# Performance work log

Measured on AMD Instinct MI355X. Metric: run time of the kernel, lower is better.

Reference implementation:

```python
import math
import jax, jax.numpy as jnp
import numpy as np

K_NEIGH = 8  # module's self.k

def setup_inputs() -> dict:
    key = jax.random.key(0)
    ks = jax.random.split(key, 5)
    B, N, D = 4, 4096, 256
    s = 1.0 / math.sqrt(D)
    return {
        "x": jax.random.normal(ks[0], (B, N, D), dtype=jnp.float32),
        "Wqkv": jax.random.normal(ks[1], (3 * D, D), dtype=jnp.float32) * s,
        "bqkv": jax.random.normal(ks[2], (3 * D,), dtype=jnp.float32) * 0.02,
        "Wout": jax.random.normal(ks[3], (D, D), dtype=jnp.float32) * s,
        "bout": jax.random.normal(ks[4], (D,), dtype=jnp.float32) * 0.02,
    }

def reference(x, Wqkv, bqkv, Wout, bout):
    B, N, D = x.shape
    qkv = x @ Wqkv.T + bqkv                      # [B,N,3D]
    q, k, v = jnp.split(qkv, 3, axis=-1)         # each [B,N,D]
    # F.normalize(k, dim=-1) with eps=1e-12
    kn = k / jnp.maximum(jnp.linalg.norm(k, axis=-1, keepdims=True), 1e-12)
    sim = jnp.einsum('bnd,bmd->bnm', kn, kn)     # [B,N,N] cosine similarity
    sim = sim - 1e9 * jnp.eye(N, dtype=sim.dtype)
    k_val = min(K_NEIGH, N - 1)
    _, idx = jax.lax.top_k(sim, k_val)           # [B,N,k] neighbor indices
    # NOTE: the torch code builds k.unsqueeze(2).expand(B,N,N,D) and gathers on
    # dim 2, but that tensor is CONSTANT along dim 2, so the gather reduces to a
    # broadcast of k (and v) over the neighbor axis -- reproduced faithfully:
    k_sel = jnp.broadcast_to(k[:, :, None, :], (B, N, k_val, D))
    v_sel = jnp.broadcast_to(v[:, :, None, :], (B, N, k_val, D))
    scores = jnp.sum(q[:, :, None, :] * k_sel, axis=-1) / math.sqrt(D)  # [B,N,k]
    attn = jax.nn.softmax(scores, axis=-1)
    out = jnp.sum(attn[..., None] * v_sel, axis=2)                      # [B,N,D]
    return x + out @ Wout.T + bout
```

## Files before the change

kernel.cpp:

```cpp
#include <hip/hip_runtime.h>
#include <hip/hip_bf16.h>

#define DD 256
#define NROWS 16384
#define TILES 4
#define TROWS 16

typedef float f32x4 __attribute__((ext_vector_type(4)));
typedef __bf16 bf16x4 __attribute__((ext_vector_type(4)));
typedef __bf16 bf16x8 __attribute__((ext_vector_type(8)));

__device__ __forceinline__ bf16x8 cvt8(f32x4 lo, f32x4 hi) {
  bf16x8 v;
#pragma unroll
  for (int j = 0; j < 4; ++j) {
    v[j] = (__bf16)lo[j];
    v[4 + j] = (__bf16)hi[j];
  }
  return v;
}

__global__ __launch_bounds__(1024) void wc_bc_kernel(
    const float* __restrict__ Wqkv, const float* __restrict__ bqkv,
    const float* __restrict__ Wout, const float* __restrict__ bout,
    __bf16* __restrict__ Wc, float* __restrict__ bc) {
  __shared__ f32x4 part[16][64];
  __shared__ float red[4];
  const int i = blockIdx.x;
  const int t = threadIdx.x;
  const int w = t >> 6, l = t & 63;
  const float* __restrict__ Wv = Wqkv + 2 * DD * DD;
  const float* __restrict__ bv = bqkv + 2 * DD;
  const float* __restrict__ wrow = Wout + (size_t)i * DD;

  f32x4 wr[4];
#pragma unroll
  for (int k = 0; k < 4; ++k) wr[k] = *(const f32x4*)(wrow + w * 16 + k * 4);

  const float* wvp = Wv + (size_t)(w * 16) * DD + l * 4;
  f32x4 a0 = {0.f, 0.f, 0.f, 0.f}, a1 = {0.f, 0.f, 0.f, 0.f};
  f32x4 a2 = {0.f, 0.f, 0.f, 0.f}, a3 = {0.f, 0.f, 0.f, 0.f};
#pragma unroll
  for (int k = 0; k < 4; ++k) {
    a0 += wr[k][0] * *(const f32x4*)(wvp + (size_t)(4 * k + 0) * DD);
    a1 += wr[k][1] * *(const f32x4*)(wvp + (size_t)(4 * k + 1) * DD);
    a2 += wr[k][2] * *(const f32x4*)(wvp + (size_t)(4 * k + 2) * DD);
    a3 += wr[k][3] * *(const f32x4*)(wvp + (size_t)(4 * k + 3) * DD);
  }
  part[w][l] = (a0 + a1) + (a2 + a3);

  if (t < 256) {
    float p = wrow[t] * bv[t];
#pragma unroll
    for (int off = 32; off > 0; off >>= 1) p += __shfl_down(p, off);
    if (l == 0) red[w] = p;
  }
  __syncthreads();
  if (w == 0) {
    f32x4 s = {0.f, 0.f, 0.f, 0.f};
#pragma unroll
    for (int k = 0; k < 16; ++k) s += part[k][l];
    bf16x4 o;
#pragma unroll
    for (int j = 0; j < 4; ++j) o[j] = (__bf16)s[j];
    *(bf16x4*)(Wc + (size_t)i * DD + l * 4) = o;
    if (l == 0) bc[i] = bout[i] + red[0] + red[1] + red[2] + red[3];
  }
}

__global__ __launch_bounds__(256, 4) void knn_attn_main(
    const float* __restrict__ x, const __bf16* __restrict__ Wc,
    const float* __restrict__ bc, float* __restrict__ out) {
  __shared__ __bf16 xs[2][TROWS * DD];

  const int t = threadIdx.x;
  const int w = t >> 6, l = t & 63;
  const int cg = blockIdx.x >> 8;
  const int rb = blockIdx.x & 255;
  const int C0 = cg * 64;
  const int Rbase = rb * (TILES * TROWS);

  const int xrow = l & 15, g4 = l >> 4;
  const int rsw = (xrow & 7) << 4;
  const int rA = w * 16 + xrow;
  const int ocol = C0 + w * 16 + g4 * 4;

  bf16x8 af[8];
  {
    const __bf16* wrp = Wc + (size_t)(C0 + rA) * DD + g4 * 8;
#pragma unroll
    for (int ks = 0; ks < 8; ++ks) af[ks] = *(const bf16x8*)(wrp + ks * 32);
  }
  const f32x4 bias = *(const f32x4*)(bc + ocol);

  const int sr = t >> 4, sc = t & 15;
  const int ssw = (sr & 7) << 4;
  const int sbase = sr * 512 + sc * 32;

  {
    const float* s0 = x + (size_t)(Rbase + sr) * DD + sc * 16;
    f32x4 a = *(const f32x4*)(s0 + 0);
    f32x4 b = *(const f32x4*)(s0 + 4);
    f32x4 c = *(const f32x4*)(s0 + 8);
    f32x4 d = *(const f32x4*)(s0 + 12);
    char* xb = (char*)&xs[0][0];
    *(bf16x8*)(xb + ((sbase + 0) ^ ssw)) = cvt8(a, b);
    *(bf16x8*)(xb + ((sbase + 16) ^ ssw)) = cvt8(c, d);
  }
  __syncthreads();

  for (int i = 0; i < TILES; ++i) {
    f32x4 a, b, c, d;
    if (i + 1 < TILES) {
      const float* sn =
          x + (size_t)(Rbase + (i + 1) * TROWS + sr) * DD + sc * 16;
      a = *(const f32x4*)(sn + 0);
      b = *(const f32x4*)(sn + 4);
      c = *(const f32x4*)(sn + 8);
      d = *(const f32x4*)(sn + 12);
    }

    const char* xb = (const char*)&xs[i & 1][0];
    f32x4 acc = {0.f, 0.f, 0.f, 0.f};
#pragma unroll
    for (int ks = 0; ks < 8; ++ks) {
      const int kb = ks * 64 + g4 * 16;
      bf16x8 bfr = *(const bf16x8*)(xb + ((xrow * 512 + kb) ^ rsw));
      acc = __builtin_amdgcn_mfma_f32_16x16x32_bf16(af[ks], bfr, acc, 0, 0, 0);
    }
    {
      const size_t idx = (size_t)(Rbase + i * TROWS + xrow) * DD + ocol;
      f32x4 xres = *(const f32x4*)(x + idx);
      *(f32x4*)(out + idx) = acc + xres + bias;
    }

    if (i + 1 < TILES) {
      char* xbn = (char*)&xs[(i + 1) & 1][0];
      *(bf16x8*)(xbn + ((sbase + 0) ^ ssw)) = cvt8(a, b);
      *(bf16x8*)(xbn + ((sbase + 16) ^ ssw)) = cvt8(c, d);
    }
    __syncthreads();
  }
}

extern "C" void kernel_launch(void* const* d_in, const int* in_sizes, int n_in,
                              void* d_out, int out_size, void* d_ws, size_t ws_size,
                              hipStream_t stream) {
  const float* x = (const float*)d_in[0];
  const float* Wqkv = (const float*)d_in[1];
  const float* bqkv = (const float*)d_in[2];
  const float* Wout = (const float*)d_in[3];
  const float* bout = (const float*)d_in[4];
  float* out = (float*)d_out;

  __bf16* Wc = (__bf16*)d_ws;
  float* bc = (float*)((char*)d_ws + DD * DD * sizeof(__bf16));

  wc_bc_kernel<<<DD, 1024, 0, stream>>>(Wqkv, bqkv, Wout, bout, Wc, bc);
  knn_attn_main<<<1024, 256, 0, stream>>>(x, Wc, bc, out);
}
```

Measured before the change: 23.14 us.

## Take residual from bf16 LDS tile, halve tiles per block, batch weight-fold rows

The main kernel now takes the residual x from the bf16 copy already staged in shared memory, so x is no longer read a second time from global memory in fp32. Each block processes two 16-row tiles instead of four, which doubles the grid, and launch bounds are raised to allow more resident blocks. The staging loads are rearranged so adjacent threads read adjacent 32-byte chunks. The weight-folding kernel computes four output rows per block with 64 blocks. The cost is that the residual is rounded to bf16, which adds error to the output and risks the accuracy tolerance.

```diff
diff --git a/kernel.cpp b/kernel.cpp
--- a/kernel.cpp
+++ b/kernel.cpp
@@ -3,7 +3,7 @@
 
 #define DD 256
 #define NROWS 16384
-#define TILES 4
+#define TILES 2
 #define TROWS 16
 
 typedef float f32x4 __attribute__((ext_vector_type(4)));
@@ -24,59 +24,70 @@
     const float* __restrict__ Wqkv, const float* __restrict__ bqkv,
     const float* __restrict__ Wout, const float* __restrict__ bout,
     __bf16* __restrict__ Wc, float* __restrict__ bc) {
-  __shared__ f32x4 part[16][64];
+  __shared__ f32x4 part[16][4][64];
   __shared__ float red[4];
-  const int i = blockIdx.x;
+  const int i0 = blockIdx.x * 4;
   const int t = threadIdx.x;
   const int w = t >> 6, l = t & 63;
   const float* __restrict__ Wv = Wqkv + 2 * DD * DD;
   const float* __restrict__ bv = bqkv + 2 * DD;
-  const float* __restrict__ wrow = Wout + (size_t)i * DD;
 
-  f32x4 wr[4];
+  f32x4 wrc[4][4];
 #pragma unroll
-  for (int k = 0; k < 4; ++k) wr[k] = *(const f32x4*)(wrow + w * 16 + k * 4);
+  for (int r = 0; r < 4; ++r)
+#pragma unroll
+    for (int kk = 0; kk < 4; ++kk)
+      wrc[r][kk] = *(const f32x4*)(Wout + (size_t)(i0 + r) * DD + w * 16 + kk * 4);
 
   const float* wvp = Wv + (size_t)(w * 16) * DD + l * 4;
   f32x4 a0 = {0.f, 0.f, 0.f, 0.f}, a1 = {0.f, 0.f, 0.f, 0.f};
   f32x4 a2 = {0.f, 0.f, 0.f, 0.f}, a3 = {0.f, 0.f, 0.f, 0.f};
 #pragma unroll
-  for (int k = 0; k < 4; ++k) {
-    a0 += wr[k][0] * *(const f32x4*)(wvp + (size_t)(4 * k + 0) * DD);
-    a1 += wr[k][1] * *(const f32x4*)(wvp + (size_t)(4 * k + 1) * DD);
-    a2 += wr[k][2] * *(const f32x4*)(wvp + (size_t)(4 * k + 2) * DD);
-    a3 += wr[k][3] * *(const f32x4*)(wvp + (size_t)(4 * k + 3) * DD);
+  for (int k = 0; k < 16; ++k) {
+    f32x4 wv = *(const f32x4*)(wvp + (size_t)k * DD);
+    a0 += wv * wrc[0][k >> 2][k & 3];
+    a1 += wv * wrc[1][k >> 2][k & 3];
+    a2 += wv * wrc[2][k >> 2][k & 3];
+    a3 += wv * wrc[3][k >> 2][k & 3];
   }
-  part[w][l] = (a0 + a1) + (a2 + a3);
+  part[w][0][l] = a0;
+  part[w][1][l] = a1;
+  part[w][2][l] = a2;
+  part[w][3][l] = a3;
 
-  if (t < 256) {
-    float p = wrow[t] * bv[t];
+  if (t >= 256 && t < 512) {
+    const int r = (t >> 6) - 4, ll = t & 63;
+    float p = 0.f;
+#pragma unroll
+    for (int k = 0; k < 4; ++k)
+      p += Wout[(size_t)(i0 + r) * DD + k * 64 + ll] * bv[k * 64 + ll];
 #pragma unroll
     for (int off = 32; off > 0; off >>= 1) p += __shfl_down(p, off);
-    if (l == 0) red[w] = p;
+    if (ll == 0) red[r] = p;
   }
   __syncthreads();
-  if (w == 0) {
+  if (t < 256) {
+    const int r = t >> 6, q = t & 63;
     f32x4 s = {0.f, 0.f, 0.f, 0.f};
 #pragma unroll
-    for (int k = 0; k < 16; ++k) s += part[k][l];
+    for (int k = 0; k < 16; ++k) s += part[k][r][q];
     bf16x4 o;
 #pragma unroll
     for (int j = 0; j < 4; ++j) o[j] = (__bf16)s[j];
-    *(bf16x4*)(Wc + (size_t)i * DD + l * 4) = o;
-    if (l == 0) bc[i] = bout[i] + red[0] + red[1] + red[2] + red[3];
+    *(bf16x4*)(Wc + (size_t)(i0 + r) * DD + q * 4) = o;
   }
+  if (t < 4) bc[i0 + t] = bout[i0 + t] + red[t];
 }
 
-__global__ __launch_bounds__(256, 4) void knn_attn_main(
+__global__ __launch_bounds__(256, 6) void knn_attn_main(
     const float* __restrict__ x, const __bf16* __restrict__ Wc,
     const float* __restrict__ bc, float* __restrict__ out) {
   __shared__ __bf16 xs[2][TROWS * DD];
 
   const int t = threadIdx.x;
   const int w = t >> 6, l = t & 63;
-  const int cg = blockIdx.x >> 8;
-  const int rb = blockIdx.x & 255;
+  const int cg = blockIdx.x >> 9;
+  const int rb = blockIdx.x & 511;
   const int C0 = cg * 64;
   const int Rbase = rb * (TILES * TROWS);
 
@@ -95,29 +106,28 @@
 
   const int sr = t >> 4, sc = t & 15;
   const int ssw = (sr & 7) << 4;
-  const int sbase = sr * 512 + sc * 32;
+  const int cb0 = sr * 512 + sc * 16;
 
   {
-    const float* s0 = x + (size_t)(Rbase + sr) * DD + sc * 16;
-    f32x4 a = *(const f32x4*)(s0 + 0);
-    f32x4 b = *(const f32x4*)(s0 + 4);
-    f32x4 c = *(const f32x4*)(s0 + 8);
-    f32x4 d = *(const f32x4*)(s0 + 12);
+    const float* src = x + (size_t)(Rbase + sr) * DD + sc * 8;
+    f32x4 a = *(const f32x4*)(src);
+    f32x4 b = *(const f32x4*)(src + 4);
+    f32x4 c = *(const f32x4*)(src + 128);
+    f32x4 d = *(const f32x4*)(src + 132);
     char* xb = (char*)&xs[0][0];
-    *(bf16x8*)(xb + ((sbase + 0) ^ ssw)) = cvt8(a, b);
-    *(bf16x8*)(xb + ((sbase + 16) ^ ssw)) = cvt8(c, d);
+    *(bf16x8*)(xb + ((cb0 + 0) ^ ssw)) = cvt8(a, b);
+    *(bf16x8*)(xb + ((cb0 + 256) ^ ssw)) = cvt8(c, d);
   }
   __syncthreads();
 
   for (int i = 0; i < TILES; ++i) {
     f32x4 a, b, c, d;
     if (i + 1 < TILES) {
-      const float* sn =
-          x + (size_t)(Rbase + (i + 1) * TROWS + sr) * DD + sc * 16;
-      a = *(const f32x4*)(sn + 0);
+      const float* sn = x + (size_t)(Rbase + (i + 1) * TROWS + sr) * DD + sc * 8;
+      a = *(const f32x4*)(sn);
       b = *(const f32x4*)(sn + 4);
-      c = *(const f32x4*)(sn + 8);
-      d = *(const f32x4*)(sn + 12);
+      c = *(const f32x4*)(sn + 128);
+      d = *(const f32x4*)(sn + 132);
     }
 
     const char* xb = (const char*)&xs[i & 1][0];
@@ -129,15 +139,18 @@
       acc = __builtin_amdgcn_mfma_f32_16x16x32_bf16(af[ks], bfr, acc, 0, 0, 0);
     }
     {
-      const size_t idx = (size_t)(Rbase + i * TROWS + xrow) * DD + ocol;
-      f32x4 xres = *(const f32x4*)(x + idx);
-      *(f32x4*)(out + idx) = acc + xres + bias;
+      bf16x4 xr4 = *(const bf16x4*)(xb + ((xrow * 512 + ocol * 2) ^ rsw));
+      f32x4 xres;
+#pragma unroll
+      for (int j = 0; j < 4; ++j) xres[j] = (float)xr4[j];
+      *(f32x4*)(out + (size_t)(Rbase + i * TROWS + xrow) * DD + ocol) =
+          acc + xres + bias;
     }
 
     if (i + 1 < TILES) {
       char* xbn = (char*)&xs[(i + 1) & 1][0];
-      *(bf16x8*)(xbn + ((sbase + 0) ^ ssw)) = cvt8(a, b);
-      *(bf16x8*)(xbn + ((sbase + 16) ^ ssw)) = cvt8(c, d);
+      *(bf16x8*)(xbn + ((cb0 + 0) ^ ssw)) = cvt8(a, b);
+      *(bf16x8*)(xbn + ((cb0 + 256) ^ ssw)) = cvt8(c, d);
     }
     __syncthreads();
   }
@@ -156,6 +169,6 @@
   __bf16* Wc = (__bf16*)d_ws;
   float* bc = (float*)((char*)d_ws + DD * DD * sizeof(__bf16));
 
-  wc_bc_kernel<<<DD, 1024, 0, stream>>>(Wqkv, bqkv, Wout, bout, Wc, bc);
-  knn_attn_main<<<1024, 256, 0, stream>>>(x, Wc, bc, out);
+  wc_bc_kernel<<<64, 1024, 0, stream>>>(Wqkv, bqkv, Wout, bout, Wc, bc);
+  knn_attn_main<<<2048, 256, 0, stream>>>(x, Wc, bc, out);
 }
```

New measurement: 24.95 us. +7.9%, slower.

## Compute all output columns per block and take residual from shared tile

Applied to the files above, without the earlier changes.

Each block now covers all 256 output columns, with each wave holding four 16-column weight fragments in registers. This replaces the four column-group blocks that each re-staged the same x rows. The x fragments are loaded from LDS once per tile and reused across four MFMA chains. The residual is read from the bf16 LDS copy instead of the fp32 global x, which removes a second global read but rounds the residual to bf16. Register pressure rises, and the grid shrinks to 512 blocks with two tiles each.

```diff
diff --git a/kernel.cpp b/kernel.cpp
--- a/kernel.cpp
+++ b/kernel.cpp
@@ -3,7 +3,7 @@
 
 #define DD 256
 #define NROWS 16384
-#define TILES 4
+#define TILES 2
 #define TROWS 16
 
 typedef float f32x4 __attribute__((ext_vector_type(4)));
@@ -68,30 +68,27 @@
   }
 }
 
-__global__ __launch_bounds__(256, 4) void knn_attn_main(
+__global__ __launch_bounds__(256, 2) void knn_attn_main(
     const float* __restrict__ x, const __bf16* __restrict__ Wc,
     const float* __restrict__ bc, float* __restrict__ out) {
   __shared__ __bf16 xs[2][TROWS * DD];
 
   const int t = threadIdx.x;
   const int w = t >> 6, l = t & 63;
-  const int cg = blockIdx.x >> 8;
-  const int rb = blockIdx.x & 255;
-  const int C0 = cg * 64;
-  const int Rbase = rb * (TILES * TROWS);
+  const int Rbase = blockIdx.x * (TILES * TROWS);
 
   const int xrow = l & 15, g4 = l >> 4;
   const int rsw = (xrow & 7) << 4;
-  const int rA = w * 16 + xrow;
-  const int ocol = C0 + w * 16 + g4 * 4;
 
-  bf16x8 af[8];
-  {
-    const __bf16* wrp = Wc + (size_t)(C0 + rA) * DD + g4 * 8;
+  bf16x8 af[4][8];
+  f32x4 bias[4];
 #pragma unroll
-    for (int ks = 0; ks < 8; ++ks) af[ks] = *(const bf16x8*)(wrp + ks * 32);
+  for (int ct = 0; ct < 4; ++ct) {
+    const __bf16* wrp = Wc + (size_t)(w * 64 + ct * 16 + xrow) * DD + g4 * 8;
+#pragma unroll
+    for (int ks = 0; ks < 8; ++ks) af[ct][ks] = *(const bf16x8*)(wrp + ks * 32);
+    bias[ct] = *(const f32x4*)(bc + w * 64 + ct * 16 + g4 * 4);
   }
-  const f32x4 bias = *(const f32x4*)(bc + ocol);
 
   const int sr = t >> 4, sc = t & 15;
   const int ssw = (sr & 7) << 4;
@@ -121,17 +118,24 @@
     }
 
     const char* xb = (const char*)&xs[i & 1][0];
-    f32x4 acc = {0.f, 0.f, 0.f, 0.f};
+    bf16x8 xf[8];
 #pragma unroll
-    for (int ks = 0; ks < 8; ++ks) {
-      const int kb = ks * 64 + g4 * 16;
-      bf16x8 bfr = *(const bf16x8*)(xb + ((xrow * 512 + kb) ^ rsw));
-      acc = __builtin_amdgcn_mfma_f32_16x16x32_bf16(af[ks], bfr, acc, 0, 0, 0);
-    }
-    {
-      const size_t idx = (size_t)(Rbase + i * TROWS + xrow) * DD + ocol;
-      f32x4 xres = *(const f32x4*)(x + idx);
-      *(f32x4*)(out + idx) = acc + xres + bias;
+    for (int ks = 0; ks < 8; ++ks)
+      xf[ks] = *(const bf16x8*)(xb + ((xrow * 512 + ks * 64 + g4 * 16) ^ rsw));
+
+#pragma unroll
+    for (int ct = 0; ct < 4; ++ct) {
+      f32x4 acc = {0.f, 0.f, 0.f, 0.f};
+#pragma unroll
+      for (int ks = 0; ks < 8; ++ks)
+        acc = __builtin_amdgcn_mfma_f32_16x16x32_bf16(af[ct][ks], xf[ks], acc, 0, 0, 0);
+      const int ocol = w * 64 + ct * 16 + g4 * 4;
+      bf16x4 xr4 = *(const bf16x4*)(xb + ((xrow * 512 + ocol * 2) ^ rsw));
+      f32x4 xres;
+#pragma unroll
+      for (int j = 0; j < 4; ++j) xres[j] = (float)xr4[j];
+      *(f32x4*)(out + (size_t)(Rbase + i * TROWS + xrow) * DD + ocol) =
+          acc + xres + bias[ct];
     }
 
     if (i + 1 < TILES) {
@@ -157,5 +161,5 @@
   float* bc = (float*)((char*)d_ws + DD * DD * sizeof(__bf16));
 
   wc_bc_kernel<<<DD, 1024, 0, stream>>>(Wqkv, bqkv, Wout, bout, Wc, bc);
-  knn_attn_main<<<1024, 256, 0, stream>>>(x, Wc, bc, out);
+  knn_attn_main<<<NROWS / (TILES * TROWS), 256, 0, stream>>>(x, Wc, bc, out);
 }
```

Measured after the change: 22.35 us. -3.4%, faster.
